# Kernel tuning notes

Hardware: AMD Instinct MI355X
Metric: run time of the kernel (lower is better)

The kernel has to match this reference:

```python
import jax, jax.numpy as jnp
import numpy as np

V, H, B, T = 32000, 1024, 32, 256  # vocab, rnn_size, batch, seq_length


def setup_inputs() -> dict:
    key = jax.random.key(0)
    ks = jax.random.split(key, 6)
    s = 1.0 / np.sqrt(H)
    return {
        "input_data": jax.random.randint(ks[0], (B, T), 0, V, dtype=jnp.int32),
        "targets": jax.random.randint(ks[1], (B, T), 0, V, dtype=jnp.int32),
        "embedding": jax.random.uniform(ks[2], (V, H), minval=-1.0, maxval=1.0, dtype=jnp.float32),
        "softmax_b": jnp.zeros((V,), jnp.float32),
        "W0": (jax.random.normal(ks[3], (2 * H, 4 * H)) * s).astype(jnp.float32),
        "b0": jnp.zeros((4 * H,), jnp.float32),
        "W1": (jax.random.normal(ks[4], (2 * H, 4 * H)) * s).astype(jnp.float32),
        "b1": jnp.zeros((4 * H,), jnp.float32),
    }


def _lstm_step(x, c, h, W, b):
    # TF LSTMCell: gates i, j, f, o; forget_bias = 1.0
    z = jnp.concatenate([x, h], axis=-1) @ W + b  # [B, 4H]
    i, j, f, o = jnp.split(z, 4, axis=-1)
    c2 = c * jax.nn.sigmoid(f + 1.0) + jax.nn.sigmoid(i) * jnp.tanh(j)
    h2 = jax.nn.sigmoid(o) * jnp.tanh(c2)
    return c2, h2


def reference(input_data, targets, embedding, softmax_b, W0, b0, W1, b1):
    x = embedding[input_data]  # [B, T, H]
    Bb, Hh = x.shape[0], embedding.shape[1]
    zeros = jnp.zeros((Bb, Hh), x.dtype)
    init = ((zeros, zeros), (zeros, zeros))  # ((c0,h0),(c1,h1))

    def step(carry, xt):
        (c0, h0), (c1, h1) = carry
        c0, h0 = _lstm_step(xt, c0, h0, W0, b0)
        c1, h1 = _lstm_step(h0, c1, h1, W1, b1)
        return ((c0, h0), (c1, h1)), h1

    _, outs = jax.lax.scan(step, init, jnp.swapaxes(x, 0, 1))  # [T, B, H]
    output = jnp.swapaxes(outs, 0, 1).reshape(-1, Hh)  # [B*T, H]
    logits = output @ embedding.T + softmax_b  # tied softmax weights, [B*T, V]
    labels = targets.reshape(-1)
    logp = jax.nn.log_softmax(logits)
    loss = -jnp.take_along_axis(logp, labels[:, None], axis=1)[:, 0]
    cost = jnp.sum(loss) / Bb
    return logits, cost
```

## Files before the change

kernel.cpp:

```cpp
#include <hip/hip_runtime.h>
#include <hip/hip_bf16.h>

#define DEV static __device__ __forceinline__

typedef unsigned short u16;
typedef unsigned long long u64;
typedef __attribute__((ext_vector_type(8))) short short8;
typedef __attribute__((ext_vector_type(4))) float f32x4;

constexpr int V = 32000, H = 1024, B = 32, T = 256;
constexpr int BT = B * T;
constexpr int G  = 4 * H;
constexpr int NCH = V / 128;
constexpr int NWG2 = 256;
constexpr int RSTRIDE = 32 * 2048 + 2048;

constexpr size_t SZ_WT    = (size_t)G * 2048 * 2;
constexpr size_t OFF_W0T  = 0;
constexpr size_t OFF_W1T  = OFF_W0T + SZ_WT;
constexpr size_t OFF_EBF  = OFF_W1T + SZ_WT;
constexpr size_t OFF_XBF  = OFF_EBF + (size_t)V * H * 2;
constexpr size_t OFF_XP0  = OFF_XBF + (size_t)BT * H * 2;
constexpr size_t OFF_H1   = OFF_XP0 + (size_t)BT * G * 2;
constexpr size_t OFF_HSEQ = OFF_H1 + (size_t)BT * H * 2;
constexpr size_t SZ_HSEQ  = (size_t)(T + 2) * RSTRIDE * 2;
constexpr size_t OFF_SYNC = OFF_HSEQ + SZ_HSEQ;
constexpr size_t SZ_SYNC  = (size_t)2 * 256 * 128 * 4;
constexpr size_t OFF_PMAX = OFF_SYNC + SZ_SYNC;
constexpr size_t OFF_PSUM = OFF_PMAX + (size_t)BT * NCH * 4;
constexpr size_t OFF_LOSS = OFF_PSUM + (size_t)BT * NCH * 4;

DEV u16 f2bf(float x) {
  union { float f; unsigned int u; } v; v.f = x;
  unsigned int r = v.u + 0x7fffu + ((v.u >> 16) & 1u);
  return (u16)(r >> 16);
}
DEV float bf2f(u16 b) {
  union { unsigned int u; float f; } v; v.u = ((unsigned int)b) << 16;
  return v.f;
}
DEV float sigm(float x) { return 1.f / (1.f + expf(-x)); }

DEV void gload_lds16(const u16* g, u16* l) {
  __builtin_amdgcn_global_load_lds(
      (__attribute__((address_space(1))) void*)g,
      (__attribute__((address_space(3))) void*)l, 16, 0, 0);
}


__global__ void k_transpose_cvt(const float* __restrict__ in, u16* __restrict__ out,
                                int R, int C) {
  __shared__ float tile[32][33];
  int bc = blockIdx.x * 32, br = blockIdx.y * 32;
  int tx = threadIdx.x & 31, ty0 = threadIdx.x >> 5;
#pragma unroll
  for (int i = 0; i < 4; ++i) {
    int ty = ty0 + i * 8;
    tile[ty][tx] = in[(size_t)(br + ty) * C + bc + tx];
  }
  __syncthreads();
#pragma unroll
  for (int i = 0; i < 4; ++i) {
    int ty = ty0 + i * 8;
    out[(size_t)(bc + ty) * R + br + tx] = f2bf(tile[tx][ty]);
  }
}

__global__ void k_cvt_bf16(const float* __restrict__ in, u16* __restrict__ out, int n4) {
  int i = blockIdx.x * blockDim.x + threadIdx.x;
  int stride = gridDim.x * blockDim.x;
  for (; i < n4; i += stride) {
    float4 v = ((const float4*)in)[i];
    ushort4 o;
    o.x = f2bf(v.x); o.y = f2bf(v.y); o.z = f2bf(v.z); o.w = f2bf(v.w);
    ((ushort4*)out)[i] = o;
  }
}

__global__ void k_gather_x(const float* __restrict__ emb, const int* __restrict__ inp,
                           u16* __restrict__ Xbf) {
  int row = blockIdx.x;
  int t = row >> 5, b = row & 31;
  int tok = inp[b * T + t];
  const float4* src = (const float4*)(emb + (size_t)tok * H);
  ushort4* dst = (ushort4*)(Xbf + (size_t)row * H);
  float4 v = src[threadIdx.x];
  ushort4 o;
  o.x = f2bf(v.x); o.y = f2bf(v.y); o.z = f2bf(v.z); o.w = f2bf(v.w);
  dst[threadIdx.x] = o;
}

__global__ void k_zero(unsigned int* __restrict__ p, int nwords) {
  int i = blockIdx.x * blockDim.x + threadIdx.x;
  int stride = gridDim.x * blockDim.x;
  for (; i < nwords; i += stride) p[i] = 0u;
}

template <bool SM_EPI, int CMODE>
__global__ __launch_bounds__(256)
void k_gemm(const u16* __restrict__ A, int lda,
            const u16* __restrict__ Bt, int ldb,
            float* __restrict__ C, int ldc,
            const float* __restrict__ bias, int K,
            float* __restrict__ pmax, float* __restrict__ psum, int nch) {
  __shared__ alignas(16) u16 ldsA[128 * 32];
  __shared__ alignas(16) u16 ldsB[128 * 32];
  __shared__ float2 red[128][2];

  unsigned nwg = gridDim.x * gridDim.y;
  unsigned flat = blockIdx.y * gridDim.x + blockIdx.x;
  unsigned nf = (flat & 7) * (nwg >> 3) + (flat >> 3);
  unsigned bx = nf % gridDim.x, by = nf / gridDim.x;

  int tid = threadIdx.x, lane = tid & 63, w = tid >> 6;
  int row0 = by * 128, col0 = bx * 128;
  int wr = w >> 1, wc = w & 1;
  int c15 = lane & 15, q4 = lane >> 4;

  const u16* ag[2]; const u16* bg[2];
#pragma unroll
  for (int j = 0; j < 2; ++j) {
    int r = (j * 4 + w) * 16 + (lane >> 2);
    int k = (lane & 3) * 8;
    ag[j] = A + (size_t)(row0 + r) * lda + k;
    bg[j] = Bt + (size_t)(col0 + r) * ldb + k;
  }
  u16* lA0 = ldsA + (size_t)(0 + w) * 512;
  u16* lA1 = ldsA + (size_t)(4 + w) * 512;
  u16* lB0 = ldsB + (size_t)(0 + w) * 512;
  u16* lB1 = ldsB + (size_t)(4 + w) * 512;

  f32x4 acc[4][4];
#pragma unroll
  for (int m = 0; m < 4; ++m)
#pragma unroll
    for (int n = 0; n < 4; ++n) acc[m][n] = (f32x4){0.f, 0.f, 0.f, 0.f};

  int nk = K >> 5;
  for (int kk = 0; kk < nk; ++kk) {
    int kb = kk * 32;
    gload_lds16(ag[0] + kb, lA0);
    gload_lds16(ag[1] + kb, lA1);
    gload_lds16(bg[0] + kb, lB0);
    gload_lds16(bg[1] + kb, lB1);
    __syncthreads();

    short8 af[4], bfr[4];
#pragma unroll
    for (int m = 0; m < 4; ++m)
      af[m] = *(const short8*)(ldsA + (wr * 64 + m * 16 + c15) * 32 + q4 * 8);
#pragma unroll
    for (int n = 0; n < 4; ++n)
      bfr[n] = *(const short8*)(ldsB + (wc * 64 + n * 16 + c15) * 32 + q4 * 8);
#pragma unroll
    for (int m = 0; m < 4; ++m)
#pragma unroll
      for (int n = 0; n < 4; ++n)
        acc[m][n] = __builtin_amdgcn_mfma_f32_16x16x32_bf16(af[m], bfr[n], acc[m][n], 0, 0, 0);
    __syncthreads();
  }

  float bias_n[4];
#pragma unroll
  for (int n = 0; n < 4; ++n) bias_n[n] = bias[col0 + wc * 64 + n * 16 + c15];

#pragma unroll
  for (int m = 0; m < 4; ++m) {
#pragma unroll
    for (int jr = 0; jr < 4; ++jr) {
      int r_g = row0 + wr * 64 + m * 16 + q4 * 4 + jr;
      float v[4];
#pragma unroll
      for (int n = 0; n < 4; ++n) {
        int c_g = col0 + wc * 64 + n * 16 + c15;
        float val = acc[m][n][jr] + bias_n[n];
        if (CMODE == 0) {
          C[(size_t)r_g * ldc + c_g] = val;
        } else {
          int tt = r_g >> 5, bb = r_g & 31;
          int q = c_g >> 10, wgup = (c_g & 1023) >> 3, uu = c_g & 7;
          ((u16*)C)[((((size_t)tt * 128 + wgup) * 32 + bb) * 32) + q * 8 + uu] = f2bf(val);
        }
        v[n] = val;
      }
      if (SM_EPI) {
        float mx = fmaxf(fmaxf(v[0], v[1]), fmaxf(v[2], v[3]));
        float s = __expf(v[0] - mx) + __expf(v[1] - mx) + __expf(v[2] - mx) + __expf(v[3] - mx);
#pragma unroll
        for (int d = 1; d < 16; d <<= 1) {
          float mo = __shfl_xor(mx, d, 64);
          float so = __shfl_xor(s, d, 64);
          float M2 = fmaxf(mx, mo);
          s = s * __expf(mx - M2) + so * __expf(mo - M2);
          mx = M2;
        }
        if (c15 == 0) red[wr * 64 + m * 16 + q4 * 4 + jr][wc] = make_float2(mx, s);
      }
    }
  }
  if (SM_EPI) {
    __syncthreads();
    if (tid < 128) {
      float2 a = red[tid][0], b2 = red[tid][1];
      float M2 = fmaxf(a.x, b2.x);
      float S = a.y * __expf(a.x - M2) + b2.y * __expf(b2.x - M2);
      pmax[(size_t)(row0 + tid) * nch + bx] = M2;
      psum[(size_t)(row0 + tid) * nch + bx] = S;
    }
  }
}


#define RED(w_, bt_, nt_, r_, c_) red[((((w_)*2 + (bt_)) * 2 + (nt_)) * 16 + (r_)) * 16 + (c_)]

DEV void wait_flags(const int* __restrict__ fa, const int* __restrict__ fb) {
  if (threadIdx.x < 64) {
    int lane = threadIdx.x;
    while (true) {
      int ok = 1;
      if (fa) {
        int a0 = __hip_atomic_load(fa + lane,      __ATOMIC_RELAXED, __HIP_MEMORY_SCOPE_AGENT);
        int a1 = __hip_atomic_load(fa + 64 + lane, __ATOMIC_RELAXED, __HIP_MEMORY_SCOPE_AGENT);
        ok &= (a0 != 0) & (a1 != 0);
      }
      if (fb) {
        int b0 = __hip_atomic_load(fb + lane,      __ATOMIC_RELAXED, __HIP_MEMORY_SCOPE_AGENT);
        int b1 = __hip_atomic_load(fb + 64 + lane, __ATOMIC_RELAXED, __HIP_MEMORY_SCOPE_AGENT);
        ok &= (b0 != 0) & (b1 != 0);
      }
      if (__all(ok)) break;
      __builtin_amdgcn_s_sleep(2);
    }
  }
  __builtin_amdgcn_sched_barrier(0);
  __syncthreads();
}

DEV void publish_flag(int* __restrict__ word) {
  __syncthreads();
  if (threadIdx.x == 0)
    __hip_atomic_store(word, 1, __ATOMIC_RELAXED, __HIP_MEMORY_SCOPE_AGENT);
}

template <int KH, bool IS_L0>
DEV void lstm_role(const u16* __restrict__ WT,
                   const u16* __restrict__ xp0p,
                   const float* __restrict__ zb1,
                   u16* __restrict__ hseq, u16* __restrict__ H1bf,
                   int* __restrict__ f0, int* __restrict__ f1,
                   float* __restrict__ red, int wgu) {
  constexpr int KOFF = IS_L0 ? 1024 : 0;
  constexpr int KS = KH / 4;
  constexpr int NKC = KS / 32;
  int tid = threadIdx.x, lane = tid & 63, w = tid >> 6;
  int c15 = lane & 15, q4 = lane >> 4;
  int eb = tid >> 3, eu = tid & 7;

  short8 wfr[2][NKC];
#pragma unroll
  for (int nt = 0; nt < 2; ++nt) {
    int lr = nt * 16 + c15;
    const u16* rp = WT + (size_t)((lr >> 3) * 1024 + wgu * 8 + (lr & 7)) * 2048
                    + KOFF + w * KS + q4 * 8;
#pragma unroll
    for (int kc = 0; kc < NKC; ++kc)
      wfr[nt][kc] = *(const short8*)(rp + kc * 32);
  }

  float zpc[4];
  if (!IS_L0) {
#pragma unroll
    for (int q = 0; q < 4; ++q) zpc[q] = zb1[q * 1024 + wgu * 8 + eu];
  }
  float creg = 0.f;

  for (int it_t = 0; it_t < T; ++it_t) {
    int t = IS_L0 ? it_t : it_t + 1;

    float zp[4];
    if (IS_L0) {
#pragma unroll
      for (int q = 0; q < 4; ++q)
        zp[q] = bf2f(xp0p[((((size_t)t * 128 + wgu) * 32 + eb) * 32) + q * 8 + eu]);
    } else {
#pragma unroll
      for (int q = 0; q < 4; ++q) zp[q] = zpc[q];
    }

    if (IS_L0) {
      if (t >= 1) wait_flags(f0 + (size_t)(t - 1) * 128, nullptr);
    } else {
      wait_flags(f0 + (size_t)(t - 1) * 128,
                 t >= 2 ? f1 + (size_t)(t - 2) * 128 : nullptr);
    }

    const u16* hread = hseq + (size_t)t * RSTRIDE;
    f32x4 acc[2][2];
#pragma unroll
    for (int bt = 0; bt < 2; ++bt)
#pragma unroll
      for (int nt = 0; nt < 2; ++nt) acc[bt][nt] = (f32x4){0.f, 0.f, 0.f, 0.f};

#pragma unroll
    for (int kc = 0; kc < NKC; ++kc) {
      int kh = w * KS + kc * 32 + q4 * 8;
      short8 a0 = *(const short8*)(hread + (size_t)c15 * 2048 + kh);
      short8 a1 = *(const short8*)(hread + (size_t)(16 + c15) * 2048 + kh);
      acc[0][0] = __builtin_amdgcn_mfma_f32_16x16x32_bf16(a0, wfr[0][kc], acc[0][0], 0, 0, 0);
      acc[0][1] = __builtin_amdgcn_mfma_f32_16x16x32_bf16(a0, wfr[1][kc], acc[0][1], 0, 0, 0);
      acc[1][0] = __builtin_amdgcn_mfma_f32_16x16x32_bf16(a1, wfr[0][kc], acc[1][0], 0, 0, 0);
      acc[1][1] = __builtin_amdgcn_mfma_f32_16x16x32_bf16(a1, wfr[1][kc], acc[1][1], 0, 0, 0);
    }

#pragma unroll
    for (int bt = 0; bt < 2; ++bt)
#pragma unroll
      for (int nt = 0; nt < 2; ++nt)
#pragma unroll
        for (int jr = 0; jr < 4; ++jr)
          RED(w, bt, nt, q4 * 4 + jr, c15) = acc[bt][nt][jr];
    __syncthreads();

    int bt = eb >> 4, rr = eb & 15;
    float z[4];
#pragma unroll
    for (int q = 0; q < 4; ++q) {
      int lr = q * 8 + eu, nt = lr >> 4, cc = lr & 15;
      z[q] = RED(0, bt, nt, rr, cc) + RED(1, bt, nt, rr, cc) +
             RED(2, bt, nt, rr, cc) + RED(3, bt, nt, rr, cc) + zp[q];
    }
    float gi = sigm(z[0]);
    float gj = tanhf(z[1]);
    float gf = sigm(z[2] + 1.f);
    float go = sigm(z[3]);
    creg = creg * gf + gi * gj;
    float hv = go * tanhf(creg);

    int hb = (int)f2bf(hv);
    int hp = __shfl_xor(hb, 1, 64);
    if (!(tid & 1)) {
      unsigned int pack = (unsigned int)(u16)hb | ((unsigned int)(u16)hp << 16);
      u16* hwr = hseq + (size_t)(t + 1) * RSTRIDE + (IS_L0 ? 0 : 1024);
      __hip_atomic_store((unsigned int*)(hwr + (size_t)eb * 2048 + wgu * 8 + eu), pack,
                         __ATOMIC_RELAXED, __HIP_MEMORY_SCOPE_AGENT);
      if (!IS_L0)
        *(unsigned int*)(H1bf + ((size_t)eb * T + (t - 1)) * H + wgu * 8 + eu) = pack;
    }

    publish_flag(IS_L0 ? (f0 + (size_t)t * 128 + wgu)
                       : (f1 + (size_t)(t - 1) * 128 + wgu));
  }
}

__global__ __launch_bounds__(256, 1)
void k_lstm_persistent(const u16* __restrict__ W0T, const u16* __restrict__ W1T,
                       const u16* __restrict__ xp0p, const float* __restrict__ b1,
                       u16* __restrict__ hseq, u16* __restrict__ H1bf,
                       int* __restrict__ sync) {
  __shared__ float red[4 * 2 * 2 * 16 * 16];
  int* f0 = sync;
  int* f1 = sync + 256 * 128;
  int wg = blockIdx.x;
  if (wg < 128)
    lstm_role<1024, true>(W0T, xp0p, nullptr, hseq, H1bf, f0, f1, red, wg);
  else
    lstm_role<2048, false>(W1T, nullptr, b1, hseq, H1bf, f0, f1, red, wg - 128);
}

__global__ void k_rowfin(const float* __restrict__ pmax, const float* __restrict__ psum,
                         const float* __restrict__ Cl, const int* __restrict__ targets,
                         float* __restrict__ loss) {
  int row = blockIdx.x;
  int tid = threadIdx.x, lane = tid & 63, w = tid >> 6;
  float mx = -1e30f, s = 0.f;
  if (tid < NCH) { mx = pmax[(size_t)row * NCH + tid]; s = psum[(size_t)row * NCH + tid]; }
#pragma unroll
  for (int d = 1; d < 64; d <<= 1) {
    float mo = __shfl_xor(mx, d, 64);
    float so = __shfl_xor(s, d, 64);
    float M2 = fmaxf(mx, mo);
    s = s * __expf(mx - M2) + so * __expf(mo - M2);
    mx = M2;
  }
  __shared__ float2 wred[4];
  if (lane == 0) wred[w] = make_float2(mx, s);
  __syncthreads();
  if (tid == 0) {
    float M = wred[0].x, S = wred[0].y;
#pragma unroll
    for (int i = 1; i < 4; ++i) {
      float M2 = fmaxf(M, wred[i].x);
      S = S * __expf(M - M2) + wred[i].y * __expf(wred[i].x - M2);
      M = M2;
    }
    float logZ = M + logf(S);
    int tgt = targets[row];
    float xt = Cl[(size_t)row * V + tgt];
    loss[row] = logZ - xt;
  }
}

__global__ void k_cost(const float* __restrict__ loss, float* __restrict__ out) {
  int tid = threadIdx.x, lane = tid & 63, w = tid >> 6;
  float s = 0.f;
  for (int i = tid; i < BT; i += 256) s += loss[i];
#pragma unroll
  for (int d = 1; d < 64; d <<= 1) s += __shfl_xor(s, d, 64);
  __shared__ float ws4[4];
  if (lane == 0) ws4[w] = s;
  __syncthreads();
  if (tid == 0) out[0] = (ws4[0] + ws4[1] + ws4[2] + ws4[3]) * (1.0f / B);
}

extern "C" void kernel_launch(void* const* d_in, const int* in_sizes, int n_in,
                              void* d_out, int out_size, void* d_ws, size_t ws_size,
                              hipStream_t stream) {
  const int*   input_data = (const int*)d_in[0];
  const int*   targets    = (const int*)d_in[1];
  const float* emb        = (const float*)d_in[2];
  const float* softmax_b  = (const float*)d_in[3];
  const float* W0         = (const float*)d_in[4];
  const float* b0         = (const float*)d_in[5];
  const float* W1         = (const float*)d_in[6];
  const float* b1         = (const float*)d_in[7];
  float* out = (float*)d_out;
  char*  ws  = (char*)d_ws;

  u16*   W0T  = (u16*)(ws + OFF_W0T);
  u16*   W1T  = (u16*)(ws + OFF_W1T);
  u16*   Ebf  = (u16*)(ws + OFF_EBF);
  u16*   Xbf  = (u16*)(ws + OFF_XBF);
  u16*   xp0p = (u16*)(ws + OFF_XP0);
  u16*   H1bf = (u16*)(ws + OFF_H1);
  u16*   hseq = (u16*)(ws + OFF_HSEQ);
  int*   sync = (int*)(ws + OFF_SYNC);
  float* pmax = (float*)(ws + OFF_PMAX);
  float* psum = (float*)(ws + OFF_PSUM);
  float* lossb= (float*)(ws + OFF_LOSS);

  k_transpose_cvt<<<dim3(G / 32, 2048 / 32), 256, 0, stream>>>(W0, W0T, 2048, G);
  k_transpose_cvt<<<dim3(G / 32, 2048 / 32), 256, 0, stream>>>(W1, W1T, 2048, G);
  k_cvt_bf16<<<2048, 256, 0, stream>>>(emb, Ebf, V * H / 4);
  k_gather_x<<<BT, 256, 0, stream>>>(emb, input_data, Xbf);
  k_zero<<<64, 256, 0, stream>>>((unsigned int*)(ws + OFF_HSEQ), RSTRIDE);
  k_zero<<<64, 256, 0, stream>>>((unsigned int*)(ws + OFF_SYNC), (int)(SZ_SYNC / 4));

  k_gemm<false, 1><<<dim3(G / 128, BT / 128), 256, 0, stream>>>(
      Xbf, H, W0T, 2048, (float*)xp0p, G, b0, H, nullptr, nullptr, 0);

  k_lstm_persistent<<<dim3(NWG2), dim3(256), 0, stream>>>(
      W0T, W1T, xp0p, b1, hseq, H1bf, sync);

  k_gemm<true, 0><<<dim3(V / 128, BT / 128), 256, 0, stream>>>(
      H1bf, H, Ebf, H, out, V, softmax_b, H, pmax, psum, NCH);

  k_rowfin<<<BT, 256, 0, stream>>>(pmax, psum, out, targets, lossb);
  k_cost<<<1, 256, 0, stream>>>(lossb, out + (size_t)BT * V);
}
```

Measured before the change: 2.997 ms.

## Use 256x256 pipelined GEMM for tied-softmax logits with swizzled LDS

Adds a new 512-thread GEMM kernel with 256x256 output tiles for the vocab projection. It uses direct global-to-LDS loads into double-buffered, XOR-swizzled tiles, runs several loads ahead of compute, and raises wave priority around MFMA bursts. The softmax partial-max/sum epilogue now merges four column partials per row, and NCH is halved to match. Larger tiles cut repeated operand loads from global memory but use more registers and LDS per workgroup. The LSTM loop also shortens its flag-poll sleep and writes H1 with nontemporal stores.

```diff
diff --git a/kernel.cpp b/kernel.cpp
--- a/kernel.cpp
+++ b/kernel.cpp
@@ -11,7 +11,7 @@
 constexpr int V = 32000, H = 1024, B = 32, T = 256;
 constexpr int BT = B * T;
 constexpr int G  = 4 * H;
-constexpr int NCH = V / 128;
+constexpr int NCH = V / 256;
 constexpr int NWG2 = 256;
 constexpr int RSTRIDE = 32 * 2048 + 2048;
 
@@ -96,16 +96,14 @@
   for (; i < nwords; i += stride) p[i] = 0u;
 }
 
-template <bool SM_EPI, int CMODE>
+template <int CMODE>
 __global__ __launch_bounds__(256)
 void k_gemm(const u16* __restrict__ A, int lda,
             const u16* __restrict__ Bt, int ldb,
             float* __restrict__ C, int ldc,
-            const float* __restrict__ bias, int K,
-            float* __restrict__ pmax, float* __restrict__ psum, int nch) {
+            const float* __restrict__ bias, int K) {
   __shared__ alignas(16) u16 ldsA[128 * 32];
   __shared__ alignas(16) u16 ldsB[128 * 32];
-  __shared__ float2 red[128][2];
 
   unsigned nwg = gridDim.x * gridDim.y;
   unsigned flat = blockIdx.y * gridDim.x + blockIdx.x;
@@ -169,7 +167,6 @@
 #pragma unroll
     for (int jr = 0; jr < 4; ++jr) {
       int r_g = row0 + wr * 64 + m * 16 + q4 * 4 + jr;
-      float v[4];
 #pragma unroll
       for (int n = 0; n < 4; ++n) {
         int c_g = col0 + wc * 64 + n * 16 + c15;
@@ -181,6 +178,131 @@
           int q = c_g >> 10, wgup = (c_g & 1023) >> 3, uu = c_g & 7;
           ((u16*)C)[((((size_t)tt * 128 + wgup) * 32 + bb) * 32) + q * 8 + uu] = f2bf(val);
         }
+      }
+    }
+  }
+}
+
+constexpr int GNT = 32;
+
+DEV void stage_half256(const u16* __restrict__ A, int lda,
+                       const u16* __restrict__ Bt, int ldb,
+                       int row0, int col0, u16* lds, int Hh, int tid) {
+  int t = Hh >> 2, j = Hh & 3, op = j >> 1, hh = j & 1;
+  int wid = tid >> 6, lane = tid & 63;
+  int r = hh * 128 + wid * 16 + (lane >> 2);
+  int k = t * 32 + (((lane & 3) ^ ((lane >> 2) & 3)) << 3);
+  const u16* g = (op == 0) ? (A + (size_t)(row0 + r) * lda + k)
+                           : (Bt + (size_t)(col0 + r) * ldb + k);
+  u16* l = lds + (size_t)((op * 2 + (t & 1)) * 8192 + (hh * 128 + wid * 16) * 32);
+  gload_lds16(g, l);
+}
+
+template <bool SM_EPI>
+__global__ __launch_bounds__(512)
+void k_gemm256(const u16* __restrict__ A, int lda,
+               const u16* __restrict__ Bt, int ldb,
+               float* __restrict__ C, int ldc,
+               const float* __restrict__ bias,
+               float* __restrict__ pmax, float* __restrict__ psum, int nch) {
+  __shared__ alignas(16) u16 lds[4 * 8192];
+
+  unsigned nwg = gridDim.x * gridDim.y;
+  unsigned flat = blockIdx.y * gridDim.x + blockIdx.x;
+  unsigned nf = (flat & 7) * (nwg >> 3) + (flat >> 3);
+  int bx = nf % gridDim.x, by = nf / gridDim.x;
+  int row0 = by * 256, col0 = bx * 256;
+
+  int tid = threadIdx.x, lane = tid & 63, wid = tid >> 6;
+  int wr = wid >> 2, wc = wid & 3;
+  int c15 = lane & 15, q4 = lane >> 4;
+  int usw = (q4 ^ (c15 & 3)) << 3;
+
+  f32x4 acc[8][4];
+#pragma unroll
+  for (int m = 0; m < 8; ++m)
+#pragma unroll
+    for (int n = 0; n < 4; ++n) acc[m][n] = (f32x4){0.f, 0.f, 0.f, 0.f};
+
+#pragma unroll
+  for (int h = 0; h < 7; ++h)
+    stage_half256(A, lda, Bt, ldb, row0, col0, lds, h, tid);
+  asm volatile("s_waitcnt vmcnt(3)" ::: "memory");
+  __builtin_amdgcn_sched_barrier(0);
+  __builtin_amdgcn_s_barrier();
+
+  int Hh = 7;
+  short8 af[4], bfr[4];
+
+  for (int t = 0; t < GNT; ++t) {
+    int pt = t & 1;
+    const u16* la = lds + pt * 8192;
+    const u16* lb = lds + (2 + pt) * 8192;
+
+#pragma unroll
+    for (int m = 0; m < 4; ++m)
+      af[m] = *(const short8*)(la + (wr * 128 + m * 16 + c15) * 32 + usw);
+#pragma unroll
+    for (int n = 0; n < 4; ++n)
+      bfr[n] = *(const short8*)(lb + (wc * 64 + n * 16 + c15) * 32 + usw);
+    if (Hh < 4 * GNT) { stage_half256(A, lda, Bt, ldb, row0, col0, lds, Hh, tid); ++Hh; }
+    if (Hh < 4 * GNT) { stage_half256(A, lda, Bt, ldb, row0, col0, lds, Hh, tid); ++Hh; }
+    __builtin_amdgcn_s_barrier();
+    asm volatile("s_waitcnt lgkmcnt(0)" ::: "memory");
+    __builtin_amdgcn_sched_barrier(0);
+    __builtin_amdgcn_s_setprio(1);
+#pragma unroll
+    for (int m = 0; m < 4; ++m)
+#pragma unroll
+      for (int n = 0; n < 4; ++n)
+        acc[m][n] = __builtin_amdgcn_mfma_f32_16x16x32_bf16(af[m], bfr[n], acc[m][n], 0, 0, 0);
+    __builtin_amdgcn_s_setprio(0);
+    __builtin_amdgcn_s_barrier();
+
+#pragma unroll
+    for (int m = 0; m < 4; ++m)
+      af[m] = *(const short8*)(la + (wr * 128 + (m + 4) * 16 + c15) * 32 + usw);
+    if (Hh < 4 * GNT) { stage_half256(A, lda, Bt, ldb, row0, col0, lds, Hh, tid); ++Hh; }
+    if (Hh < 4 * GNT) { stage_half256(A, lda, Bt, ldb, row0, col0, lds, Hh, tid); ++Hh; }
+    __builtin_amdgcn_s_barrier();
+    asm volatile("s_waitcnt lgkmcnt(0)" ::: "memory");
+    __builtin_amdgcn_sched_barrier(0);
+    __builtin_amdgcn_s_setprio(1);
+#pragma unroll
+    for (int m = 0; m < 4; ++m)
+#pragma unroll
+      for (int n = 0; n < 4; ++n)
+        acc[m + 4][n] = __builtin_amdgcn_mfma_f32_16x16x32_bf16(af[m], bfr[n], acc[m + 4][n], 0, 0, 0);
+    __builtin_amdgcn_s_setprio(0);
+    if (t < GNT - 2) {
+      asm volatile("s_waitcnt vmcnt(3)" ::: "memory");
+      __builtin_amdgcn_sched_barrier(0);
+    } else if (t == GNT - 2) {
+      asm volatile("s_waitcnt vmcnt(0)" ::: "memory");
+      __builtin_amdgcn_sched_barrier(0);
+    }
+    __builtin_amdgcn_s_barrier();
+  }
+
+  float bias_n[4];
+#pragma unroll
+  for (int n = 0; n < 4; ++n) bias_n[n] = bias[col0 + wc * 64 + n * 16 + c15];
+
+  float2* red = (float2*)lds;
+  __syncthreads();
+
+#pragma unroll
+  for (int m = 0; m < 8; ++m) {
+#pragma unroll
+    for (int jr = 0; jr < 4; ++jr) {
+      int rloc = wr * 128 + m * 16 + q4 * 4 + jr;
+      int r_g = row0 + rloc;
+      float v[4];
+#pragma unroll
+      for (int n = 0; n < 4; ++n) {
+        int c_g = col0 + wc * 64 + n * 16 + c15;
+        float val = acc[m][n][jr] + bias_n[n];
+        C[(size_t)r_g * ldc + c_g] = val;
         v[n] = val;
       }
       if (SM_EPI) {
@@ -194,17 +316,22 @@
           s = s * __expf(mx - M2) + so * __expf(mo - M2);
           mx = M2;
         }
-        if (c15 == 0) red[wr * 64 + m * 16 + q4 * 4 + jr][wc] = make_float2(mx, s);
+        if (c15 == 0) red[rloc * 4 + wc] = make_float2(mx, s);
       }
     }
   }
   if (SM_EPI) {
     __syncthreads();
-    if (tid < 128) {
-      float2 a = red[tid][0], b2 = red[tid][1];
-      float M2 = fmaxf(a.x, b2.x);
-      float S = a.y * __expf(a.x - M2) + b2.y * __expf(b2.x - M2);
-      pmax[(size_t)(row0 + tid) * nch + bx] = M2;
+    if (tid < 256) {
+      float M = -1e30f, S = 0.f;
+#pragma unroll
+      for (int i = 0; i < 4; ++i) {
+        float2 a = red[tid * 4 + i];
+        float M2 = fmaxf(M, a.x);
+        S = S * __expf(M - M2) + a.y * __expf(a.x - M2);
+        M = M2;
+      }
+      pmax[(size_t)(row0 + tid) * nch + bx] = M;
       psum[(size_t)(row0 + tid) * nch + bx] = S;
     }
   }
@@ -229,7 +356,7 @@
         ok &= (b0 != 0) & (b1 != 0);
       }
       if (__all(ok)) break;
-      __builtin_amdgcn_s_sleep(2);
+      __builtin_amdgcn_s_sleep(1);
     }
   }
   __builtin_amdgcn_sched_barrier(0);
@@ -344,7 +471,8 @@
       __hip_atomic_store((unsigned int*)(hwr + (size_t)eb * 2048 + wgu * 8 + eu), pack,
                          __ATOMIC_RELAXED, __HIP_MEMORY_SCOPE_AGENT);
       if (!IS_L0)
-        *(unsigned int*)(H1bf + ((size_t)eb * T + (t - 1)) * H + wgu * 8 + eu) = pack;
+        __builtin_nontemporal_store(pack,
+            (unsigned int*)(H1bf + ((size_t)eb * T + (t - 1)) * H + wgu * 8 + eu));
     }
 
     publish_flag(IS_L0 ? (f0 + (size_t)t * 128 + wgu)
@@ -445,14 +573,14 @@
   k_zero<<<64, 256, 0, stream>>>((unsigned int*)(ws + OFF_HSEQ), RSTRIDE);
   k_zero<<<64, 256, 0, stream>>>((unsigned int*)(ws + OFF_SYNC), (int)(SZ_SYNC / 4));
 
-  k_gemm<false, 1><<<dim3(G / 128, BT / 128), 256, 0, stream>>>(
-      Xbf, H, W0T, 2048, (float*)xp0p, G, b0, H, nullptr, nullptr, 0);
+  k_gemm<1><<<dim3(G / 128, BT / 128), 256, 0, stream>>>(
+      Xbf, H, W0T, 2048, (float*)xp0p, G, b0, H);
 
   k_lstm_persistent<<<dim3(NWG2), dim3(256), 0, stream>>>(
       W0T, W1T, xp0p, b1, hseq, H1bf, sync);
 
-  k_gemm<true, 0><<<dim3(V / 128, BT / 128), 256, 0, stream>>>(
-      H1bf, H, Ebf, H, out, V, softmax_b, H, pmax, psum, NCH);
+  k_gemm256<true><<<dim3(V / 256, BT / 256), 512, 0, stream>>>(
+      H1bf, H, Ebf, H, out, V, softmax_b, pmax, psum, NCH);
 
   k_rowfin<<<BT, 256, 0, stream>>>(pmax, psum, out, targets, lossb);
   k_cost<<<1, 256, 0, stream>>>(lossb, out + (size_t)BT * V);
```

Result: no change. 2.991 ms (-0.2%).
